# Performance work log

Hardware: AMD Instinct MI355X
Metric: run time of the kernel (lower is better)

The kernel has to match this reference:

```python
import jax, jax.numpy as jnp
import numpy as np
import itertools, math

CUTOFF = 10.0
ON_CUT = 0.25 * CUTOFF
OFF_CUT = 0.75 * CUTOFF
ALPHA = 4.0 / CUTOFF + 0.001
ALPHA2 = ALPHA ** 2
TWO_PI = 2.0 * math.pi
ONE_OVER_SQRTPI = 1.0 / math.sqrt(math.pi)
B = 512      # molecules
NA = 128     # atoms per molecule
N = B * NA   # total atoms
DEG = 64     # neighbors per atom
P = N * DEG  # total pairs


def _make_kvecs(Nmax=(2, 2, 2)):
    ks = []
    for i in range(3):
        kk = list(range(Nmax[i] + 1)) + [-v for v in range(1, Nmax[i] + 1)]
        ks.append(kk)
    lk = list(itertools.product(*ks))[1:]  # drop (0,0,0)
    kv = np.array(lk, dtype=np.float32)
    kmax = max(Nmax)
    return jnp.asarray(kv[(kv ** 2).sum(-1) <= kmax ** 2])  # [32,3]


def setup_inputs() -> dict:
    key = jax.random.key(0)
    k1, k2, k3, k4, k5, k6 = jax.random.split(key, 6)
    Z = jax.random.randint(k1, (N,), 1, 94)
    Qa = 0.2 * jax.random.normal(k2, (N,), dtype=jnp.float32)
    R = 20.0 * jax.random.uniform(k3, (N, 3), dtype=jnp.float32)
    Dij = 0.5 + 9.5 * jax.random.uniform(k4, (P,), dtype=jnp.float32)
    idx_i = jnp.repeat(jnp.arange(N), DEG)
    idx_j = (idx_i // NA) * NA + jax.random.randint(k5, (P,), 0, NA)
    batch_seg = jnp.repeat(jnp.arange(B), NA)
    Cell = jnp.tile(20.0 * jnp.eye(3, dtype=jnp.float32), (B, 1, 1)) \
           + 0.05 * jax.random.normal(k6, (B, 3, 3), dtype=jnp.float32)
    kvecs = _make_kvecs()
    return dict(Dij=Dij, Qa=Qa, R=R, Cell=Cell, kvecs=kvecs,
                Z=Z, idx_i=idx_i, idx_j=idx_j, batch_seg=batch_seg)


def _switch_function(x):
    # infinitely smooth switch from 1 (x<=on) to 0 (x>=off)
    def comp(t):
        t_ = jnp.where(t <= 0, 1.0, t)
        return jnp.where(t <= 0, 0.0, jnp.exp(-1.0 / t_))
    x = (x - ON_CUT) / (OFF_CUT - ON_CUT)
    fp = comp(x)
    fm = comp(1.0 - x)
    return jnp.where(x <= 0, 1.0, jnp.where(x >= 1, 0.0, fm / (fp + fm)))


def reference(Dij, Qa, R, Cell, kvecs, Z, idx_i, idx_j, batch_seg):
    # ---- real space: gather -> elementwise -> segment_sum ----
    fac = Qa[idx_i] * Qa[idx_j]                              # [P]
    f = _switch_function(Dij)
    coulomb = 1.0 / Dij
    damped = 1.0 / jnp.sqrt(Dij * Dij + 1.0)
    pw = fac * (f * damped + (1.0 - f) * coulomb) * jax.lax.erfc(ALPHA * Dij)
    e_real = 0.5 * jax.ops.segment_sum(pw, idx_i, num_segments=N)  # [N]

    # ---- reciprocal space ----
    recip_box = TWO_PI * jnp.transpose(jnp.linalg.inv(Cell), (0, 2, 1))  # [B,3,3]
    v_box = jnp.abs(jnp.linalg.det(Cell))                    # [B]
    prefactor = TWO_PI / v_box                               # [B]
    k = jnp.einsum('kx,bxy->bky', kvecs, recip_box)          # [B,K,3]
    k2 = jnp.sum(k * k, axis=-1)                             # [B,K]
    qg = jnp.exp(-0.25 * k2 / ALPHA2)                        # [B,K]
    kd = jnp.einsum('nkx,nx->nk', k[batch_seg], R)           # [N,K]
    q_real = jax.ops.segment_sum(Qa[:, None] * jnp.cos(kd), batch_seg, num_segments=B)  # [B,K]
    q_imag = jax.ops.segment_sum(Qa[:, None] * jnp.sin(kd), batch_seg, num_segments=B)  # [B,K]
    q_dens = q_real ** 2 + q_imag ** 2
    # NOTE: faithful to TF source: reduce over ALL axes -> scalar, then * prefactor [B]
    e_reciprocal = prefactor * jnp.sum(q_dens * qg / k2)     # [B]
    e_self = -ALPHA * ONE_OVER_SQRTPI * jax.ops.segment_sum(Qa * Qa, batch_seg, num_segments=B)
    QaR = jax.ops.segment_sum(Qa[:, None] * R, batch_seg, num_segments=B)  # [B,3]
    e_bc = prefactor / 3.0 * jnp.sum(QaR * QaR, axis=-1)     # [B]
    e_rec_tot = e_reciprocal + e_self + e_bc                 # [B]

    Na_per_batch = jax.ops.segment_sum(jnp.ones_like(batch_seg, dtype=Qa.dtype),
                                       batch_seg, num_segments=B)
    er = (e_rec_tot / Na_per_batch)[batch_seg]               # per-atom broadcast [N]
    return e_real + er, Qa
```

## Files before the change

kernel.cpp:

```cpp
#include <hip/hip_runtime.h>
#include <math.h>

#define ON_CUT_C   2.5f
#define OFF_CUT_C  7.5f
#define ALPHA_C    0.401f
#define ALPHA2_C   0.160801f
#define TWO_PI_C   6.2831853071795864f
#define INV_SQRT_PI_C 0.56418958354775628f
#define NB   512
#define NA_C 128
#define NTOT (NB*NA_C)
#define DEG_C 64
#define KC   32

#define RCP(x) __builtin_amdgcn_rcpf(x)
#define RSQ(x) __builtin_amdgcn_rsqf(x)

__device__ __forceinline__ float fast_erfc(float x) {
    float t = RCP(1.0f + 0.3275911f * x);
    float p = t*(0.254829592f + t*(-0.284496736f +
              t*(1.421413741f + t*(-1.453152027f + t*1.061405429f))));
    return p * __expf(-x*x);
}

__global__ __launch_bounds__(256) void recip_batch_kernel(
    const float* __restrict__ Qa, const float* __restrict__ R,
    const float* __restrict__ Cell, const float* __restrict__ kvecs,
    float* __restrict__ ws)
{
    int b   = blockIdx.x;
    int tid = threadIdx.x;

    __shared__ float sqa[NA_C], srx[NA_C], sry[NA_C], srz[NA_C];
    __shared__ float skx[KC], sky[KC], skz[KC], sgok2[KC];
    __shared__ float pr[KC][9], pi[KC][9];
    __shared__ float redw[2][4];
    __shared__ float s_pref;

    if (tid < NA_C) {
        int n = b * NA_C + tid;
        sqa[tid] = Qa[n];
        srx[tid] = R[n*3+0]; sry[tid] = R[n*3+1]; srz[tid] = R[n*3+2];
    }
    if (tid < KC) {
        const float* C = Cell + b * 9;
        float c00=C[0], c01=C[1], c02=C[2];
        float c10=C[3], c11=C[4], c12=C[5];
        float c20=C[6], c21=C[7], c22=C[8];
        float m00 = c11*c22 - c12*c21;
        float m01 = c02*c21 - c01*c22;
        float m02 = c01*c12 - c02*c11;
        float m10 = c12*c20 - c10*c22;
        float m11 = c00*c22 - c02*c20;
        float m12 = c02*c10 - c00*c12;
        float m20 = c10*c21 - c11*c20;
        float m21 = c01*c20 - c00*c21;
        float m22 = c00*c11 - c01*c10;
        float det = c00*m00 + c01*m10 + c02*m20;
        float invdet = 1.0f / det;
        float kv0 = kvecs[tid*3+0], kv1 = kvecs[tid*3+1], kv2 = kvecs[tid*3+2];
        float kx = TWO_PI_C * invdet * (m00*kv0 + m01*kv1 + m02*kv2);
        float ky = TWO_PI_C * invdet * (m10*kv0 + m11*kv1 + m12*kv2);
        float kz = TWO_PI_C * invdet * (m20*kv0 + m21*kv1 + m22*kv2);
        float k2 = kx*kx + ky*ky + kz*kz;
        skx[tid] = kx; sky[tid] = ky; skz[tid] = kz;
        sgok2[tid] = __expf(-0.25f * k2 / ALPHA2_C) / k2;
        if (tid == 0) s_pref = TWO_PI_C / fabsf(det);
    }
    __syncthreads();

    int k = tid & 31, chunk = tid >> 5;
    float kx = skx[k], ky = sky[k], kz = skz[k];
    float cr = 0.0f, ci = 0.0f;
    int a0 = chunk * 16;
    #pragma unroll
    for (int i = 0; i < 16; ++i) {
        int a = a0 + i;
        float kd = kx*srx[a] + ky*sry[a] + kz*srz[a];
        float s, c;
        __sincosf(kd, &s, &c);
        cr += sqa[a] * c;
        ci += sqa[a] * s;
    }
    pr[k][chunk] = cr; pi[k][chunk] = ci;

    if (tid < NA_C) {
        float qa = sqa[tid], rx = srx[tid], ry = sry[tid], rz = srz[tid];
        float q2 = qa*qa, px = qa*rx, py = qa*ry, pz = qa*rz;
        #pragma unroll
        for (int off = 32; off; off >>= 1) {
            q2 += __shfl_down(q2, off, 64);
            px += __shfl_down(px, off, 64);
            py += __shfl_down(py, off, 64);
            pz += __shfl_down(pz, off, 64);
        }
        if ((tid & 63) == 0) {
            int w = tid >> 6;
            redw[w][0]=q2; redw[w][1]=px; redw[w][2]=py; redw[w][3]=pz;
        }
    }
    __syncthreads();

    if (tid < KC) {
        float r = 0.0f, im = 0.0f;
        #pragma unroll
        for (int c = 0; c < 8; ++c) { r += pr[tid][c]; im += pi[tid][c]; }
        float sterm = (r*r + im*im) * sgok2[tid];
        #pragma unroll
        for (int off = 16; off; off >>= 1) sterm += __shfl_down(sterm, off, 64);
        if (tid == 0) {
            ws[b] = sterm;
            float pref = s_pref;
            float q2t = redw[0][0] + redw[1][0];
            float X = redw[0][1] + redw[1][1];
            float Y = redw[0][2] + redw[1][2];
            float Zc = redw[0][3] + redw[1][3];
            ws[NB + b] = pref;
            ws[2*NB + b] = -ALPHA_C * INV_SQRT_PI_C * q2t
                           + (pref * (1.0f/3.0f)) * (X*X + Y*Y + Zc*Zc);
        }
    }
}

__global__ __launch_bounds__(256) void real_final_kernel(
    const float* __restrict__ Dij, const float* __restrict__ Qa,
    const int* __restrict__ idx_j, const float* __restrict__ ws,
    float* __restrict__ out)
{
    int tid   = threadIdx.x;
    int wave  = blockIdx.x * 4 + (tid >> 6);
    int lane  = tid & 63;
    int g     = lane >> 4;
    int il    = lane & 15;
    int atom  = wave * 4 + g;
    int p     = atom * DEG_C + il * 4;

    __shared__ float s_er;

    if (tid < 64) {
        float s = 0.0f;
        #pragma unroll
        for (int i = 0; i < 8; ++i) s += ws[tid + 64*i];
        #pragma unroll
        for (int off = 32; off; off >>= 1) s += __shfl_xor(s, off, 64);
        if (tid == 0) {
            int b = (blockIdx.x * 16) >> 7;
            s_er = (ws[NB + b] * s + ws[2*NB + b]) * (1.0f / NA_C);
        }
    }

    float4 D4 = *(const float4*)(Dij + p);
    int4   j4 = *(const int4*)(idx_j + p);
    float  qi = Qa[atom];

    float Dv[4] = {D4.x, D4.y, D4.z, D4.w};
    int   jv[4] = {j4.x, j4.y, j4.z, j4.w};

    float pw = 0.0f;
    #pragma unroll
    for (int e = 0; e < 4; ++e) {
        float D  = Dv[e];
        float qj = Qa[jv[e]];
        float x  = (D - ON_CUT_C) * (1.0f / (OFF_CUT_C - ON_CUT_C));
        float xc = fminf(fmaxf(x, 1e-12f), 0.99999994f);
        float gg = RCP(1.0f - xc) - RCP(xc);
        float f  = RCP(1.0f + __expf(gg));
        float coulomb = RCP(D);
        float damped  = RSQ(D*D + 1.0f);
        pw += (qi * qj) * (f*damped + (1.0f - f)*coulomb) * fast_erfc(ALPHA_C * D);
    }

    #pragma unroll
    for (int off = 8; off; off >>= 1) pw += __shfl_xor(pw, off, 64);

    __syncthreads();

    if (il == 0) {
        out[atom]        = 0.5f * pw + s_er;
        out[NTOT + atom] = qi;
    }
}

extern "C" void kernel_launch(void* const* d_in, const int* in_sizes, int n_in,
                              void* d_out, int out_size, void* d_ws, size_t ws_size,
                              hipStream_t stream) {
    const float* Dij   = (const float*)d_in[0];
    const float* Qa    = (const float*)d_in[1];
    const float* R     = (const float*)d_in[2];
    const float* Cell  = (const float*)d_in[3];
    const float* kvecs = (const float*)d_in[4];
    const int*   idx_j = (const int*)d_in[7];
    float* ws  = (float*)d_ws;
    float* out = (float*)d_out;

    recip_batch_kernel<<<NB, 256, 0, stream>>>(Qa, R, Cell, kvecs, ws);
    real_final_kernel<<<NTOT/16, 256, 0, stream>>>(Dij, Qa, idx_j, ws, out);
}
```

Before: 17.73 us.

## Fuse real-space pair sum into per-molecule reciprocal kernel with tiny finalize pass

Merges the real-space pair computation into the per-molecule reciprocal kernel. Each 512-thread block handles one molecule, prefetches Dij/idx_j before the reciprocal work, and reads neighbor charges from shared memory using the molecule-local index instead of gathering from global memory. A small finalize kernel then adds the per-molecule reciprocal term to the output with a read-modify-write. This removes the global Qa gathers and overlaps the streaming loads with the k-space math. The trade-offs are an extra pass over the output, higher register pressure from 16 prefetched pairs per thread, and reliance on idx_j always pointing within the same molecule.

Result: faster. 17.13 us (-3.4%).

```diff
diff --git a/kernel.cpp b/kernel.cpp
--- a/kernel.cpp
+++ b/kernel.cpp
@@ -23,17 +23,18 @@
     return p * __expf(-x*x);
 }
 
-__global__ __launch_bounds__(256) void recip_batch_kernel(
-    const float* __restrict__ Qa, const float* __restrict__ R,
-    const float* __restrict__ Cell, const float* __restrict__ kvecs,
-    float* __restrict__ ws)
+__global__ __launch_bounds__(512, 4) void ewald_fused_kernel(
+    const float* __restrict__ Dij, const float* __restrict__ Qa,
+    const float* __restrict__ R, const float* __restrict__ Cell,
+    const float* __restrict__ kvecs, const int* __restrict__ idx_j,
+    float* __restrict__ ws, float* __restrict__ out)
 {
     int b   = blockIdx.x;
     int tid = threadIdx.x;
 
     __shared__ float sqa[NA_C], srx[NA_C], sry[NA_C], srz[NA_C];
     __shared__ float skx[KC], sky[KC], skz[KC], sgok2[KC];
-    __shared__ float pr[KC][9], pi[KC][9];
+    __shared__ float pr[KC][17], pi[KC][17];
     __shared__ float redw[2][4];
     __shared__ float s_pref;
 
@@ -42,6 +43,18 @@
         sqa[tid] = Qa[n];
         srx[tid] = R[n*3+0]; sry[tid] = R[n*3+1]; srz[tid] = R[n*3+2];
     }
+
+    int atom_l = tid >> 2;
+    int il     = tid & 3;
+    const float* Dp = Dij + ((size_t)(b * NA_C + atom_l) * DEG_C + il * 16);
+    const int*   Jp = idx_j + ((size_t)(b * NA_C + atom_l) * DEG_C + il * 16);
+    float4 D4[4]; int4 J4[4];
+    #pragma unroll
+    for (int c = 0; c < 4; ++c) {
+        D4[c] = *(const float4*)(Dp + c * 4);
+        J4[c] = *(const int4*)(Jp + c * 4);
+    }
+
     if (tid < KC) {
         const float* C = Cell + b * 9;
         float c00=C[0], c01=C[1], c02=C[2];
@@ -69,20 +82,22 @@
     }
     __syncthreads();
 
-    int k = tid & 31, chunk = tid >> 5;
-    float kx = skx[k], ky = sky[k], kz = skz[k];
-    float cr = 0.0f, ci = 0.0f;
-    int a0 = chunk * 16;
-    #pragma unroll
-    for (int i = 0; i < 16; ++i) {
-        int a = a0 + i;
-        float kd = kx*srx[a] + ky*sry[a] + kz*srz[a];
-        float s, c;
-        __sincosf(kd, &s, &c);
-        cr += sqa[a] * c;
-        ci += sqa[a] * s;
-    }
-    pr[k][chunk] = cr; pi[k][chunk] = ci;
+    {
+        int k = tid & 31, chunk = tid >> 5;
+        float kx = skx[k], ky = sky[k], kz = skz[k];
+        float cr = 0.0f, ci = 0.0f;
+        int a0 = chunk * 8;
+        #pragma unroll
+        for (int i = 0; i < 8; ++i) {
+            int a = a0 + i;
+            float kd = kx*srx[a] + ky*sry[a] + kz*srz[a];
+            float s, c;
+            __sincosf(kd, &s, &c);
+            cr += sqa[a] * c;
+            ci += sqa[a] * s;
+        }
+        pr[k][chunk] = cr; pi[k][chunk] = ci;
+    }
 
     if (tid < NA_C) {
         float qa = sqa[tid], rx = srx[tid], ry = sry[tid], rz = srz[tid];
@@ -104,37 +119,53 @@
     if (tid < KC) {
         float r = 0.0f, im = 0.0f;
         #pragma unroll
-        for (int c = 0; c < 8; ++c) { r += pr[tid][c]; im += pi[tid][c]; }
+        for (int c = 0; c < 16; ++c) { r += pr[tid][c]; im += pi[tid][c]; }
         float sterm = (r*r + im*im) * sgok2[tid];
         #pragma unroll
         for (int off = 16; off; off >>= 1) sterm += __shfl_down(sterm, off, 64);
         if (tid == 0) {
             ws[b] = sterm;
-            float pref = s_pref;
             float q2t = redw[0][0] + redw[1][0];
-            float X = redw[0][1] + redw[1][1];
-            float Y = redw[0][2] + redw[1][2];
+            float X  = redw[0][1] + redw[1][1];
+            float Y  = redw[0][2] + redw[1][2];
             float Zc = redw[0][3] + redw[1][3];
-            ws[NB + b] = pref;
+            ws[NB + b] = s_pref;
             ws[2*NB + b] = -ALPHA_C * INV_SQRT_PI_C * q2t
-                           + (pref * (1.0f/3.0f)) * (X*X + Y*Y + Zc*Zc);
-        }
-    }
-}
-
-__global__ __launch_bounds__(256) void real_final_kernel(
-    const float* __restrict__ Dij, const float* __restrict__ Qa,
-    const int* __restrict__ idx_j, const float* __restrict__ ws,
-    float* __restrict__ out)
+                           + (s_pref * (1.0f/3.0f)) * (X*X + Y*Y + Zc*Zc);
+        }
+    }
+
+    float qi = sqa[atom_l];
+    float pw = 0.0f;
+    #pragma unroll
+    for (int c = 0; c < 4; ++c) {
+        float Dv[4] = {D4[c].x, D4[c].y, D4[c].z, D4[c].w};
+        int   jv[4] = {J4[c].x, J4[c].y, J4[c].z, J4[c].w};
+        #pragma unroll
+        for (int e = 0; e < 4; ++e) {
+            float D  = Dv[e];
+            float qj = sqa[jv[e] & (NA_C - 1)];
+            float x  = (D - ON_CUT_C) * (1.0f / (OFF_CUT_C - ON_CUT_C));
+            float xc = fminf(fmaxf(x, 1e-12f), 0.99999994f);
+            float gg = RCP(1.0f - xc) - RCP(xc);
+            float f  = RCP(1.0f + __expf(gg));
+            float coulomb = RCP(D);
+            float damped  = RSQ(D*D + 1.0f);
+            pw += (qi * qj) * (f*damped + (1.0f - f)*coulomb) * fast_erfc(ALPHA_C * D);
+        }
+    }
+    pw += __shfl_xor(pw, 1, 64);
+    pw += __shfl_xor(pw, 2, 64);
+    if (il == 0) out[b * NA_C + atom_l] = 0.5f * pw;
+
+    if (tid < NA_C) out[NTOT + b * NA_C + tid] = sqa[tid];
+}
+
+__global__ __launch_bounds__(128) void finalize_kernel(
+    const float* __restrict__ ws, float* __restrict__ out)
 {
-    int tid   = threadIdx.x;
-    int wave  = blockIdx.x * 4 + (tid >> 6);
-    int lane  = tid & 63;
-    int g     = lane >> 4;
-    int il    = lane & 15;
-    int atom  = wave * 4 + g;
-    int p     = atom * DEG_C + il * 4;
-
+    int b   = blockIdx.x;
+    int tid = threadIdx.x;
     __shared__ float s_er;
 
     if (tid < 64) {
@@ -143,42 +174,13 @@
         for (int i = 0; i < 8; ++i) s += ws[tid + 64*i];
         #pragma unroll
         for (int off = 32; off; off >>= 1) s += __shfl_xor(s, off, 64);
-        if (tid == 0) {
-            int b = (blockIdx.x * 16) >> 7;
+        if (tid == 0)
             s_er = (ws[NB + b] * s + ws[2*NB + b]) * (1.0f / NA_C);
-        }
-    }
-
-    float4 D4 = *(const float4*)(Dij + p);
-    int4   j4 = *(const int4*)(idx_j + p);
-    float  qi = Qa[atom];
-
-    float Dv[4] = {D4.x, D4.y, D4.z, D4.w};
-    int   jv[4] = {j4.x, j4.y, j4.z, j4.w};
-
-    float pw = 0.0f;
-    #pragma unroll
-    for (int e = 0; e < 4; ++e) {
-        float D  = Dv[e];
-        float qj = Qa[jv[e]];
-        float x  = (D - ON_CUT_C) * (1.0f / (OFF_CUT_C - ON_CUT_C));
-        float xc = fminf(fmaxf(x, 1e-12f), 0.99999994f);
-        float gg = RCP(1.0f - xc) - RCP(xc);
-        float f  = RCP(1.0f + __expf(gg));
-        float coulomb = RCP(D);
-        float damped  = RSQ(D*D + 1.0f);
-        pw += (qi * qj) * (f*damped + (1.0f - f)*coulomb) * fast_erfc(ALPHA_C * D);
-    }
-
-    #pragma unroll
-    for (int off = 8; off; off >>= 1) pw += __shfl_xor(pw, off, 64);
-
+    }
     __syncthreads();
 
-    if (il == 0) {
-        out[atom]        = 0.5f * pw + s_er;
-        out[NTOT + atom] = qi;
-    }
+    int n = b * NA_C + tid;
+    out[n] += s_er;
 }
 
 extern "C" void kernel_launch(void* const* d_in, const int* in_sizes, int n_in,
@@ -193,6 +195,6 @@
     float* ws  = (float*)d_ws;
     float* out = (float*)d_out;
 
-    recip_batch_kernel<<<NB, 256, 0, stream>>>(Qa, R, Cell, kvecs, ws);
-    real_final_kernel<<<NTOT/16, 256, 0, stream>>>(Dij, Qa, idx_j, ws, out);
-}
+    ewald_fused_kernel<<<NB, 512, 0, stream>>>(Dij, Qa, R, Cell, kvecs, idx_j, ws, out);
+    finalize_kernel<<<NB, NA_C, 0, stream>>>(ws, out);
+}
```
